# Performance work log

Hardware: AMD Instinct MI355X
Metric: run time of the kernel (lower is better)

Reference implementation:

```python
import jax, jax.numpy as jnp
import numpy as np

LEN_M = 131328   # (data_dim+1) * d_h = 513 * 256
D_H = 256
N_MC = 64
DATA_DIM_P1 = 513
N = 4096


def setup_inputs() -> dict:
    key = jax.random.key(0)
    k1, k2, k3, k4 = jax.random.split(key, 4)
    params = jax.random.normal(k1, (2 * LEN_M,), dtype=jnp.float32)
    W1 = jax.random.normal(k2, (D_H + 1,), dtype=jnp.float32)
    x = jax.random.normal(k3, (N, DATA_DIM_P1), dtype=jnp.float32)
    eps = jax.random.normal(k4, (N_MC,), dtype=jnp.float32)
    return {"params": params, "W1": W1, "x": x, "eps": eps}


def reference(params, W1, x, eps):
    # split variational params into means and (relu'd) variances
    m_w0 = params[:LEN_M]                                  # [len_m]
    v_w0 = jax.nn.relu(params[LEN_M:]) + 1e-6              # [len_m]
    # reparameterized MC sampling; NOTE: torch code draws ONE scalar eps per
    # MC sample (randn(m_w0[0].shape) is scalar), shared across all weights.
    samps_w0 = m_w0[:, None] + eps[None, :] * jnp.sqrt(v_w0)[:, None]  # [len_m, M]
    W0 = samps_w0.reshape(DATA_DIM_P1, D_H, N_MC)          # [d+1, h, M]
    # fused batched GEMM replacing the d_h * num_MC_samps tiny matmuls
    x_w0 = jnp.einsum('nd,dhm->nhm', x, W0)                # [N, h, M]
    z = jax.nn.relu(x_w0)
    ones = jnp.ones((x.shape[0], 1, N_MC), dtype=x.dtype)
    z = jnp.concatenate([ones, z], axis=1)                 # [N, h+1, M]
    pred_samps = jnp.einsum('nhm,h->nm', z, W1)            # [N, M]
    return pred_samps, m_w0, v_w0
```

## Files before the change

kernel.cpp:

```cpp
#include <hip/hip_runtime.h>
#include <hip/hip_bf16.h>
#include <math.h>

#define LEN_M   131328
#define D_P1    513
#define NROW    4096
#define PRED_ELEMS (NROW * 64)

typedef __attribute__((ext_vector_type(8))) short short8;
typedef __attribute__((ext_vector_type(4))) float floatx4;
typedef __attribute__((ext_vector_type(2))) float v2f;

__device__ __forceinline__ void gl_lds16(const void* g, void* l)
{
    __builtin_amdgcn_global_load_lds(
        (const __attribute__((address_space(1))) unsigned int*)g,
        (__attribute__((address_space(3))) unsigned int*)l, 16, 0, 0);
}

__device__ __forceinline__ unsigned short bf16b(float f)
{
    __hip_bfloat16 h = __float2bfloat16(f);
    return *(unsigned short*)&h;
}

__global__ __launch_bounds__(256) void prep_kernel(
    const float* __restrict__ params, float* __restrict__ out,
    __hip_bfloat16* __restrict__ wcbt)
{
    __shared__ unsigned short T[64][65];
    const int bid = blockIdx.x;
    const int t   = threadIdx.x;

    if (bid < 1024) {
        int i = bid * 256 + t;
        out[i] = 0.0f;
        if (i < LEN_M) {
            float m = params[i];
            float v = fmaxf(params[LEN_M + i], 0.0f) + 1e-6f;
            out[PRED_ELEMS + i]         = m;
            out[PRED_ELEMS + LEN_M + i] = v;
        }
        return;
    }

    const int b2 = bid - 1024;
    const int k0 = (b2 & 7) * 64;
    const int c0 = (b2 >> 3) * 64;
    const int hh = t & 63, kb = t >> 6;
    const bool spart = (c0 >= 256);
    const int hbase = c0 & 255;
    const float* src = params + (spart ? LEN_M : 0);

    #pragma unroll 4
    for (int p = 0; p < 16; ++p) {
        int kk = p * 4 + kb;
        float v = src[(k0 + kk) * 256 + hbase + hh];
        if (spart) v = sqrtf(fmaxf(v, 0.0f) + 1e-6f);
        T[kk][hh] = bf16b(v);
    }
    __syncthreads();

    const int cc = t >> 2, kq = t & 3;
    short8 lo, hi;
    #pragma unroll
    for (int j = 0; j < 8; ++j) lo[j] = (short)T[kq * 16 + j][cc];
    #pragma unroll
    for (int j = 0; j < 8; ++j) hi[j] = (short)T[kq * 16 + 8 + j][cc];

    const int cR  = c0 + cc;
    const int swz = (cR >> 1) & 3;
    const int g1  = (k0 >> 3) + 2 * kq;
    const int g2  = g1 + 1;
    const int d1  = cR * 64 + (g1 & ~3) + ((g1 & 3) ^ swz);
    const int d2  = cR * 64 + (g2 & ~3) + ((g2 & 3) ^ swz);
    short* wb = (short*)wcbt;
    *(short8*)(wb + d1 * 8) = lo;
    *(short8*)(wb + d2 * 8) = hi;
}

__global__ __launch_bounds__(256) void main_kernel(
    const __hip_bfloat16* __restrict__ wcbt, const float* __restrict__ params,
    const float* __restrict__ x, const float* __restrict__ W1,
    const float* __restrict__ eps, float* __restrict__ out)
{
    __shared__ char smem[49152];
    char*  Bs   = smem;
    char*  As   = smem + 16384;
    float* Clds = (float*)(smem + 16384);

    const int t = threadIdx.x;
    const int w4 = t >> 6, lane = t & 63;
    const int lane15 = lane & 15, quad = lane >> 4;
    const int H  = blockIdx.x;
    const int bm = blockIdx.y * 32;

    const short* wb = (const short*)wcbt;
    const short* bsrc0; const short* bsrc1;
    {
        int ch0 = t, ch1 = 256 + t;
        int lc0 = ch0 >> 2, qs0 = ch0 & 3;
        int lc1 = ch1 >> 2, qs1 = ch1 & 3;
        int c0g = H * 64 + lc0 + ((lc0 >> 6) * 192);
        int c1g = H * 64 + lc1 + ((lc1 >> 6) * 192);
        bsrc0 = wb + (c0g * 64 + qs0) * 8;
        bsrc1 = wb + (c1g * 64 + qs1) * 8;
    }
    char* bd0 = Bs + t * 16;
    char* bd1 = Bs + 4096 + t * 16;

    gl_lds16(bsrc0, bd0);
    gl_lds16(bsrc1, bd1);

    {
        const int ar = t >> 3, a8 = t & 7;
        const float* axp = x + (bm + ar) * D_P1;
        unsigned short* arow = (unsigned short*)As + ar * 512;
        #pragma unroll 4
        for (int ks = 0; ks < 16; ++ks) {
            int k = ks * 32 + a8 * 4;
            float f0 = axp[k], f1 = axp[k + 1], f2 = axp[k + 2], f3 = axp[k + 3];
            int chunk = k >> 3;
            int half  = a8 & 1;
            int cs = (chunk & ~7) | ((chunk & 7) ^ (ar & 7));
            ushort4 pk;
            pk.x = bf16b(f0); pk.y = bf16b(f1); pk.z = bf16b(f2); pk.w = bf16b(f3);
            *(ushort4*)(arow + cs * 8 + half * 4) = pk;
        }
    }

    const float e = eps[lane];
    float xl[2][4];
    #pragma unroll
    for (int rh = 0; rh < 2; ++rh)
        #pragma unroll
        for (int i = 0; i < 4; ++i)
            xl[rh][i] = x[(bm + rh * 16 + quad * 4 + i) * D_P1 + 512];
    float wl[2];
    #pragma unroll
    for (int s = 0; s < 2; ++s) {
        int lc = w4 * 32 + s * 16 + lane15;
        int c  = H * 64 + lc + ((lc >> 6) * 192);
        wl[s] = (c < 256) ? params[131072 + c]
                          : sqrtf(fmaxf(params[LEN_M + 131072 + (c - 256)], 0.0f) + 1e-6f);
    }

    int bfo[2];
    #pragma unroll
    for (int s = 0; s < 2; ++s) {
        int lc = w4 * 32 + s * 16 + lane15;
        bfo[s] = lc * 64 + ((quad ^ ((lc >> 1) & 3)) * 16);
    }
    const int ax7 = lane15 & 7;

    floatx4 acc00 = {0.f,0.f,0.f,0.f}, acc01 = acc00, acc10 = acc00, acc11 = acc00;

    __syncthreads();

    for (int ks = 0; ks < 16; ++ks) {
        const int nb = (ks + 1) & 1;
        gl_lds16(bsrc0 + (ks + 1) * 32, bd0 + nb * 8192);
        gl_lds16(bsrc1 + (ks + 1) * 32, bd1 + nb * 8192);

        const int cs16 = ((ks >> 1) * 8 + (((ks & 1) * 4 + quad) ^ ax7)) * 16;
        short8 a0 = *(const short8*)(As + lane15 * 1024 + cs16);
        short8 a1 = *(const short8*)(As + (16 + lane15) * 1024 + cs16);
        const char* Bb = Bs + (ks & 1) * 8192;
        short8 b0 = *(const short8*)(Bb + bfo[0]);
        short8 b1 = *(const short8*)(Bb + bfo[1]);

        acc00 = __builtin_amdgcn_mfma_f32_16x16x32_bf16(a0, b0, acc00, 0, 0, 0);
        acc01 = __builtin_amdgcn_mfma_f32_16x16x32_bf16(a0, b1, acc01, 0, 0, 0);
        acc10 = __builtin_amdgcn_mfma_f32_16x16x32_bf16(a1, b0, acc10, 0, 0, 0);
        acc11 = __builtin_amdgcn_mfma_f32_16x16x32_bf16(a1, b1, acc11, 0, 0, 0);
        __syncthreads();
    }

    floatx4 accs[2][2] = {{acc00, acc01}, {acc10, acc11}};
    #pragma unroll
    for (int rh = 0; rh < 2; ++rh)
        #pragma unroll
        for (int s = 0; s < 2; ++s) {
            float4 o;
            o.x = accs[rh][s][0] + xl[rh][0] * wl[s];
            o.y = accs[rh][s][1] + xl[rh][1] * wl[s];
            o.z = accs[rh][s][2] + xl[rh][2] * wl[s];
            o.w = accs[rh][s][3] + xl[rh][3] * wl[s];
            int lc = w4 * 32 + s * 16 + lane15;
            int r0 = rh * 16 + quad * 4;
            *(float4*)&Clds[lc * 36 + r0] = o;
        }
    __syncthreads();

    const int rb = w4 * 8;
    const float binit = (H == 0) ? W1[0] : 0.0f;
    v2f accp[4];
    #pragma unroll
    for (int j = 0; j < 4; ++j) accp[j] = (v2f){binit, binit};
    const v2f e2 = {e, e};
    const v2f z2 = {0.f, 0.f};

    #pragma unroll 4
    for (int lh = 0; lh < 64; ++lh) {
        const float w1h = W1[1 + H * 64 + lh];
        const v2f w2 = {w1h, w1h};
        const v2f* ap = (const v2f*)&Clds[lh * 36 + rb];
        const v2f* bp = (const v2f*)&Clds[(64 + lh) * 36 + rb];
        #pragma unroll
        for (int j = 0; j < 4; ++j) {
            v2f t2 = __builtin_elementwise_fma(e2, bp[j], ap[j]);
            t2 = __builtin_elementwise_max(t2, z2);
            accp[j] = __builtin_elementwise_fma(t2, w2, accp[j]);
        }
    }

    float* op = out + (bm + rb) * 64 + lane;
    #pragma unroll
    for (int j = 0; j < 4; ++j) {
        unsafeAtomicAdd(op + (2 * j) * 64,     accp[j].x);
        unsafeAtomicAdd(op + (2 * j + 1) * 64, accp[j].y);
    }
}

extern "C" void kernel_launch(void* const* d_in, const int* in_sizes, int n_in,
                              void* d_out, int out_size, void* d_ws, size_t ws_size,
                              hipStream_t stream)
{
    const float* params = (const float*)d_in[0];
    const float* W1     = (const float*)d_in[1];
    const float* x      = (const float*)d_in[2];
    const float* eps    = (const float*)d_in[3];
    float* out = (float*)d_out;
    __hip_bfloat16* wcbt = (__hip_bfloat16*)d_ws;

    prep_kernel<<<1024 + 64, 256, 0, stream>>>(params, out, wcbt);
    main_kernel<<<dim3(4, 128), 256, 0, stream>>>(wcbt, params, x, W1, eps, out);
}
```

Before: 84.83 us.

## Fuse prep and GEMM kernels into one cooperative launch with grid sync

Merges the weight-transpose/prep kernel and the main GEMM kernel into a single cooperative kernel of 512 blocks. The first 64 blocks build the bf16 swizzled weight buffer while the rest zero the output and copy the mean/variance outputs. All blocks stage their x tile before a grid-wide sync, then run the MFMA GEMM and reduction. This removes one kernel launch and the gap between the two kernels, and overlaps x staging with the prep work. In exchange it adds a grid barrier and cooperative-launch overhead, and requires every block to be co-resident.

```diff
diff --git a/kernel.cpp b/kernel.cpp
--- a/kernel.cpp
+++ b/kernel.cpp
@@ -1,6 +1,9 @@
 #include <hip/hip_runtime.h>
+#include <hip/hip_cooperative_groups.h>
 #include <hip/hip_bf16.h>
 #include <math.h>
+
+namespace cg = cooperative_groups;
 
 #define LEN_M   131328
 #define D_P1    513
@@ -24,93 +27,71 @@
     return *(unsigned short*)&h;
 }
 
-__global__ __launch_bounds__(256) void prep_kernel(
-    const float* __restrict__ params, float* __restrict__ out,
-    __hip_bfloat16* __restrict__ wcbt)
-{
-    __shared__ unsigned short T[64][65];
+__global__ __launch_bounds__(256) void fused_kernel(
+    const float* __restrict__ params, const float* __restrict__ x,
+    const float* __restrict__ W1, const float* __restrict__ eps,
+    float* __restrict__ out, __hip_bfloat16* __restrict__ wcbt)
+{
+    __shared__ char smem[49152];
+    char*  Bs   = smem;
+    char*  As   = smem + 16384;
+    float* Clds = (float*)(smem + 16384);
+    unsigned short (*T)[65] = (unsigned short (*)[65])smem;
+
     const int bid = blockIdx.x;
     const int t   = threadIdx.x;
-
-    if (bid < 1024) {
-        int i = bid * 256 + t;
-        out[i] = 0.0f;
-        if (i < LEN_M) {
+    const int w4 = t >> 6, lane = t & 63;
+    const int lane15 = lane & 15, quad = lane >> 4;
+    const int H  = bid & 3;
+    const int bm = (bid >> 2) * 32;
+
+    if (bid < 64) {
+        const int k0 = (bid & 7) * 64;
+        const int c0 = (bid >> 3) * 64;
+        const int hh = t & 63, kb = t >> 6;
+        const bool spart = (c0 >= 256);
+        const int hbase = c0 & 255;
+        const float* src = params + (spart ? LEN_M : 0);
+
+        #pragma unroll 4
+        for (int p = 0; p < 16; ++p) {
+            int kk = p * 4 + kb;
+            float v = src[(k0 + kk) * 256 + hbase + hh];
+            if (spart) v = sqrtf(fmaxf(v, 0.0f) + 1e-6f);
+            T[kk][hh] = bf16b(v);
+        }
+        __syncthreads();
+
+        const int cc = t >> 2, kq = t & 3;
+        short8 lo, hi;
+        #pragma unroll
+        for (int j = 0; j < 8; ++j) lo[j] = (short)T[kq * 16 + j][cc];
+        #pragma unroll
+        for (int j = 0; j < 8; ++j) hi[j] = (short)T[kq * 16 + 8 + j][cc];
+
+        const int cR  = c0 + cc;
+        const int swz = (cR >> 1) & 3;
+        const int g1  = (k0 >> 3) + 2 * kq;
+        const int g2  = g1 + 1;
+        const int d1  = cR * 64 + (g1 & ~3) + ((g1 & 3) ^ swz);
+        const int d2  = cR * 64 + (g2 & ~3) + ((g2 & 3) ^ swz);
+        short* wb = (short*)wcbt;
+        *(short8*)(wb + d1 * 8) = lo;
+        *(short8*)(wb + d2 * 8) = hi;
+        __syncthreads();
+    } else {
+        const int j = (bid - 64) * 256 + t;
+        if (j < 65536) {
+            float4 z = {0.f, 0.f, 0.f, 0.f};
+            *(float4*)(out + j * 4) = z;
+        }
+        for (int i = j; i < LEN_M; i += 448 * 256) {
             float m = params[i];
             float v = fmaxf(params[LEN_M + i], 0.0f) + 1e-6f;
             out[PRED_ELEMS + i]         = m;
             out[PRED_ELEMS + LEN_M + i] = v;
         }
-        return;
-    }
-
-    const int b2 = bid - 1024;
-    const int k0 = (b2 & 7) * 64;
-    const int c0 = (b2 >> 3) * 64;
-    const int hh = t & 63, kb = t >> 6;
-    const bool spart = (c0 >= 256);
-    const int hbase = c0 & 255;
-    const float* src = params + (spart ? LEN_M : 0);
-
-    #pragma unroll 4
-    for (int p = 0; p < 16; ++p) {
-        int kk = p * 4 + kb;
-        float v = src[(k0 + kk) * 256 + hbase + hh];
-        if (spart) v = sqrtf(fmaxf(v, 0.0f) + 1e-6f);
-        T[kk][hh] = bf16b(v);
-    }
-    __syncthreads();
-
-    const int cc = t >> 2, kq = t & 3;
-    short8 lo, hi;
-    #pragma unroll
-    for (int j = 0; j < 8; ++j) lo[j] = (short)T[kq * 16 + j][cc];
-    #pragma unroll
-    for (int j = 0; j < 8; ++j) hi[j] = (short)T[kq * 16 + 8 + j][cc];
-
-    const int cR  = c0 + cc;
-    const int swz = (cR >> 1) & 3;
-    const int g1  = (k0 >> 3) + 2 * kq;
-    const int g2  = g1 + 1;
-    const int d1  = cR * 64 + (g1 & ~3) + ((g1 & 3) ^ swz);
-    const int d2  = cR * 64 + (g2 & ~3) + ((g2 & 3) ^ swz);
-    short* wb = (short*)wcbt;
-    *(short8*)(wb + d1 * 8) = lo;
-    *(short8*)(wb + d2 * 8) = hi;
-}
-
-__global__ __launch_bounds__(256) void main_kernel(
-    const __hip_bfloat16* __restrict__ wcbt, const float* __restrict__ params,
-    const float* __restrict__ x, const float* __restrict__ W1,
-    const float* __restrict__ eps, float* __restrict__ out)
-{
-    __shared__ char smem[49152];
-    char*  Bs   = smem;
-    char*  As   = smem + 16384;
-    float* Clds = (float*)(smem + 16384);
-
-    const int t = threadIdx.x;
-    const int w4 = t >> 6, lane = t & 63;
-    const int lane15 = lane & 15, quad = lane >> 4;
-    const int H  = blockIdx.x;
-    const int bm = blockIdx.y * 32;
-
-    const short* wb = (const short*)wcbt;
-    const short* bsrc0; const short* bsrc1;
-    {
-        int ch0 = t, ch1 = 256 + t;
-        int lc0 = ch0 >> 2, qs0 = ch0 & 3;
-        int lc1 = ch1 >> 2, qs1 = ch1 & 3;
-        int c0g = H * 64 + lc0 + ((lc0 >> 6) * 192);
-        int c1g = H * 64 + lc1 + ((lc1 >> 6) * 192);
-        bsrc0 = wb + (c0g * 64 + qs0) * 8;
-        bsrc1 = wb + (c1g * 64 + qs1) * 8;
-    }
-    char* bd0 = Bs + t * 16;
-    char* bd1 = Bs + 4096 + t * 16;
-
-    gl_lds16(bsrc0, bd0);
-    gl_lds16(bsrc1, bd1);
+    }
 
     {
         const int ar = t >> 3, a8 = t & 7;
@@ -145,6 +126,26 @@
                           : sqrtf(fmaxf(params[LEN_M + 131072 + (c - 256)], 0.0f) + 1e-6f);
     }
 
+    __threadfence();
+    cg::this_grid().sync();
+
+    const short* wb = (const short*)wcbt;
+    const short* bsrc0; const short* bsrc1;
+    {
+        int ch0 = t, ch1 = 256 + t;
+        int lc0 = ch0 >> 2, qs0 = ch0 & 3;
+        int lc1 = ch1 >> 2, qs1 = ch1 & 3;
+        int c0g = H * 64 + lc0 + ((lc0 >> 6) * 192);
+        int c1g = H * 64 + lc1 + ((lc1 >> 6) * 192);
+        bsrc0 = wb + (c0g * 64 + qs0) * 8;
+        bsrc1 = wb + (c1g * 64 + qs1) * 8;
+    }
+    char* bd0 = Bs + t * 16;
+    char* bd1 = Bs + 4096 + t * 16;
+
+    gl_lds16(bsrc0, bd0);
+    gl_lds16(bsrc1, bd1);
+
     int bfo[2];
     #pragma unroll
     for (int s = 0; s < 2; ++s) {
@@ -233,6 +234,8 @@
     float* out = (float*)d_out;
     __hip_bfloat16* wcbt = (__hip_bfloat16*)d_ws;
 
-    prep_kernel<<<1024 + 64, 256, 0, stream>>>(params, out, wcbt);
-    main_kernel<<<dim3(4, 128), 256, 0, stream>>>(wcbt, params, x, W1, eps, out);
-}
+    void* args[] = {(void*)&params, (void*)&x, (void*)&W1, (void*)&eps,
+                    (void*)&out, (void*)&wcbt};
+    hipLaunchCooperativeKernel((const void*)fused_kernel, dim3(512), dim3(256),
+                               args, 0, stream);
+}
```

Result: slower. 206.8 us (+143.8%).
